# Optimization experiments

Hardware: AMD Instinct MI355X
Metric: run time of the kernel (lower is better)

## Reference

```python
import jax, jax.numpy as jnp
import numpy as np

EMBED_DIMS = 1024
NUM_HEADS = 16
HEAD_DIMS = EMBED_DIMS // NUM_HEADS


def setup_inputs() -> dict:
    key = jax.random.key(0)
    k_x, k_wqkv, k_bqkv, k_wp, k_bp = jax.random.split(key, 5)
    B, N, D = 2, 2048, EMBED_DIMS
    x = jax.random.normal(k_x, (B, N, D), dtype=jnp.float32)
    # torch nn.Linear(in, out): weight [out, in], y = x @ W.T + b
    s = 1.0 / np.sqrt(D)
    W_qkv = jax.random.uniform(k_wqkv, (3 * D, D), jnp.float32, -s, s)
    b_qkv = jax.random.uniform(k_bqkv, (3 * D,), jnp.float32, -s, s)
    W_proj = jax.random.uniform(k_wp, (D, D), jnp.float32, -s, s)
    b_proj = jax.random.uniform(k_bp, (D,), jnp.float32, -s, s)
    return {"x": x, "W_qkv": W_qkv, "b_qkv": b_qkv, "W_proj": W_proj, "b_proj": b_proj}


def reference(x, W_qkv, b_qkv, W_proj, b_proj):
    B, N, D = x.shape
    H, Hd = NUM_HEADS, HEAD_DIMS
    # qkv projection: [B, N, 3, H, Hd] -> split q, k, v as [B, H, N, Hd]
    qkv = (x @ W_qkv.T + b_qkv).reshape(B, N, 3, H, Hd).transpose(2, 0, 3, 1, 4)
    q, k, v = qkv[0], qkv[1], qkv[2]
    scale = 1.0 / jnp.sqrt(jnp.asarray(Hd, x.dtype))
    attn = jnp.einsum("bhqd,bhkd->bhqk", q, k) * scale  # [B, H, N, N]
    attn = jax.nn.softmax(attn, axis=-1)
    out = jnp.einsum("bhqk,bhkd->bhqd", attn, v)  # [B, H, N, Hd]
    out = out.transpose(0, 2, 1, 3).reshape(B, N, D)
    out = out @ W_proj.T + b_proj
    return out
```

## Files before the change

### kernel.cpp

```cpp
#include <hip/hip_runtime.h>

typedef _Float16 f16x8 __attribute__((ext_vector_type(8)));
typedef __attribute__((ext_vector_type(4))) float f32x4;

static __device__ __forceinline__ unsigned short f2h(float f) {
  return __builtin_bit_cast(unsigned short, (_Float16)f);
}

#if __has_builtin(__builtin_amdgcn_exp2f)
#define EXP2(x) __builtin_amdgcn_exp2f(x)
#else
#define EXP2(x) exp2f(x)
#endif

#define GLOAD_LDS16(gp, lp)                                          \
  __builtin_amdgcn_global_load_lds(                                  \
      (const __attribute__((address_space(1))) unsigned int*)(gp),   \
      (__attribute__((address_space(3))) unsigned int*)(lp), 16, 0, 0)

__global__ __launch_bounds__(256) void cvt_all(
    const float* __restrict__ X, const float* __restrict__ Wq,
    const float* __restrict__ Wp, unsigned short* __restrict__ Xb,
    unsigned short* __restrict__ Wqb, unsigned short* __restrict__ Wpb) {
  const int i = blockIdx.x * 256 + threadIdx.x;
  const float4* src;
  unsigned short* dst;
  int off;
  if (i < 1048576) {
    src = (const float4*)X; dst = Xb; off = i;
  } else if (i < 1835008) {
    src = (const float4*)Wq; dst = Wqb; off = i - 1048576;
  } else {
    src = (const float4*)Wp; dst = Wpb; off = i - 1835008;
  }
  const float4 v = src[off];
  *(ushort4*)(dst + (size_t)off * 4) =
      make_ushort4(f2h(v.x), f2h(v.y), f2h(v.z), f2h(v.w));
}

__global__ __launch_bounds__(512) void qkv_gemm(
    const unsigned short* __restrict__ Xb, const unsigned short* __restrict__ Wb,
    const float* __restrict__ bias, unsigned short* __restrict__ Qb,
    unsigned short* __restrict__ Kb, unsigned short* __restrict__ Vt) {
  __shared__ __align__(16) unsigned short A_sh[2][128 * 32];
  __shared__ __align__(16) unsigned short B_sh[2][128 * 32];
  const int n0 = blockIdx.x * 128, m0 = blockIdx.y * 128;
  const int tid = threadIdx.x, lane = tid & 63, wave = tid >> 6;
  const int wr = wave >> 1, wc = wave & 1;
  const int lm = lane & 15, lg = lane >> 4;
  const int r4 = lane >> 2;
  const int sg8 = (((lane & 3) ^ ((r4 >> 1) & 3)) * 8);
  const int lgx = (lg ^ ((lm >> 1) & 3)) * 8;

  f32x4 acc[2][4] = {};

#define QSTAGE(k0_, b_)                                                       \
  do {                                                                        \
    if (wave < 4) {                                                           \
      _Pragma("unroll")                                                       \
      for (int j = 0; j < 2; ++j) {                                           \
        const int chunk = wave * 2 + j;                                       \
        const int row = chunk * 16 + r4;                                      \
        GLOAD_LDS16(Xb + (size_t)(m0 + row) * 1024 + (k0_) + sg8,             \
                    &A_sh[b_][chunk * 512]);                                  \
      }                                                                       \
    } else {                                                                  \
      _Pragma("unroll")                                                       \
      for (int j = 0; j < 2; ++j) {                                           \
        const int chunk = (wave - 4) * 2 + j;                                 \
        const int row = chunk * 16 + r4;                                      \
        GLOAD_LDS16(Wb + (size_t)(n0 + row) * 1024 + (k0_) + sg8,             \
                    &B_sh[b_][chunk * 512]);                                  \
      }                                                                       \
    }                                                                         \
  } while (0)

  QSTAGE(0, 0);

  for (int it = 0; it < 32; ++it) {
    const int cur = it & 1;
    __syncthreads();
    if (it < 31) QSTAGE((it + 1) * 32, cur ^ 1);

    f16x8 af[2], bfr[4];
#pragma unroll
    for (int mi = 0; mi < 2; ++mi)
      af[mi] = *(const f16x8*)&A_sh[cur][(wr * 32 + mi * 16 + lm) * 32 + lgx];
#pragma unroll
    for (int ni = 0; ni < 4; ++ni)
      bfr[ni] = *(const f16x8*)&B_sh[cur][(wc * 64 + ni * 16 + lm) * 32 + lgx];
#pragma unroll
    for (int mi = 0; mi < 2; ++mi)
#pragma unroll
      for (int ni = 0; ni < 4; ++ni)
        acc[mi][ni] = __builtin_amdgcn_mfma_f32_16x16x32_f16(
            af[mi], bfr[ni], acc[mi][ni], 0, 0, 0);
  }
#undef QSTAGE

  const float qscale = 0.18033688011112042f;
#pragma unroll
  for (int mi = 0; mi < 2; ++mi) {
#pragma unroll
    for (int ni = 0; ni < 4; ++ni) {
      const int gn = n0 + wc * 64 + ni * 16 + lm;
      const float bv = bias[gn];
      const int which = gn >> 10;
      const int h = (gn >> 6) & 15;
      const int hd = gn & 63;
      float v[4];
#pragma unroll
      for (int r = 0; r < 4; ++r) v[r] = acc[mi][ni][r] + bv;
      const int gm0 = m0 + wr * 32 + mi * 16 + lg * 4;
      const int bb = gm0 >> 11;
      const int nq0 = gm0 & 2047;
      if (which == 0) {
        unsigned short* p = Qb + (((size_t)bb * 16 + h) * 2048 + nq0) * 64 + hd;
        p[0] = f2h(v[0] * qscale);   p[64] = f2h(v[1] * qscale);
        p[128] = f2h(v[2] * qscale); p[192] = f2h(v[3] * qscale);
      } else if (which == 1) {
        unsigned short* p = Kb + (((size_t)bb * 16 + h) * 2048 + nq0) * 64 + hd;
        p[0] = f2h(v[0]);   p[64] = f2h(v[1]);
        p[128] = f2h(v[2]); p[192] = f2h(v[3]);
      } else {
        *(ushort4*)(Vt + (((size_t)bb * 16 + h) * 64 + hd) * 2048 + nq0) =
            make_ushort4(f2h(v[0]), f2h(v[1]), f2h(v[2]), f2h(v[3]));
      }
    }
  }
}

__global__ __launch_bounds__(512) void attn_kernel(
    const unsigned short* __restrict__ Qb, const unsigned short* __restrict__ Kb,
    const unsigned short* __restrict__ Vt, unsigned short* __restrict__ Ob) {
  __shared__ __align__(16) unsigned short K_sh[2][2][64 * 32];
  __shared__ __align__(16) unsigned short V_sh[2][2][64 * 32];
  __shared__ __align__(16) unsigned short P_sh[128 * 68];
  const int bh = blockIdx.y, q0 = blockIdx.x * 128;
  const size_t base = (size_t)bh * (2048 * 64);
  const unsigned short* Qp = Qb + base;
  const unsigned short* Kp = Kb + base;
  const unsigned short* Vp = Vt + base;
  const int tid = threadIdx.x, lane = tid & 63, wave = tid >> 6;
  const int lm = lane & 15, lg = lane >> 4;
  const int r4 = lane >> 2;
  const int sg8 = (((lane & 3) ^ ((r4 >> 1) & 3)) * 8);
  const int lgx = (lg ^ ((lm >> 1) & 3)) * 8;

  f16x8 qf[2];
#pragma unroll
  for (int kc = 0; kc < 2; ++kc)
    qf[kc] = *(const f16x8*)(Qp +
        (size_t)(q0 + wave * 16 + lm) * 64 + kc * 32 + lg * 8);

  f32x4 o[4] = {};
  float lsum[4] = {};

  const bool isV = wave >= 4;
  const int plane = wave & 1;
  const int half = (wave >> 1) & 1;

#define STAGE(kt_, b_)                                                        \
  do {                                                                        \
    if (!isV) {                                                               \
      _Pragma("unroll")                                                       \
      for (int qv = 0; qv < 2; ++qv)                                          \
        GLOAD_LDS16(Kp + (size_t)((kt_) * 64 + half * 32 + qv * 16 + r4) * 64 \
                        + plane * 32 + sg8,                                   \
                    &K_sh[b_][plane][(half * 2 + qv) * 512]);                 \
    } else {                                                                  \
      _Pragma("unroll")                                                       \
      for (int qv = 0; qv < 2; ++qv)                                          \
        GLOAD_LDS16(Vp + (size_t)(half * 32 + qv * 16 + r4) * 2048 +          \
                        (kt_) * 64 + plane * 32 + sg8,                        \
                    &V_sh[b_][plane][(half * 2 + qv) * 512]);                 \
    }                                                                         \
  } while (0)

  STAGE(0, 0);

  for (int kt = 0; kt < 32; ++kt) {
    const int cur = kt & 1;
    __syncthreads();
    if (kt < 31) STAGE(kt + 1, cur ^ 1);

    f32x4 s[4] = {};
#pragma unroll
    for (int kc = 0; kc < 2; ++kc) {
#pragma unroll
      for (int ni = 0; ni < 4; ++ni) {
        const f16x8 kf =
            *(const f16x8*)&K_sh[cur][kc][(ni * 16 + lm) * 32 + lgx];
        s[ni] = __builtin_amdgcn_mfma_f32_16x16x32_f16(qf[kc], kf, s[ni], 0, 0, 0);
      }
    }

#pragma unroll
    for (int ni = 0; ni < 4; ++ni) {
      float p0 = EXP2(s[ni][0]), p1 = EXP2(s[ni][1]);
      float p2 = EXP2(s[ni][2]), p3 = EXP2(s[ni][3]);
      lsum[0] += p0; lsum[1] += p1; lsum[2] += p2; lsum[3] += p3;
      unsigned short* pp = &P_sh[(wave * 16 + lg * 4) * 68 + ni * 16 + lm];
      pp[0] = f2h(p0);    pp[68] = f2h(p1);
      pp[136] = f2h(p2);  pp[204] = f2h(p3);
    }

#pragma unroll
    for (int kc = 0; kc < 2; ++kc) {
      const f16x8 pa =
          *(const f16x8*)&P_sh[(wave * 16 + lm) * 68 + kc * 32 + lg * 8];
#pragma unroll
      for (int ni = 0; ni < 4; ++ni) {
        const f16x8 vb =
            *(const f16x8*)&V_sh[cur][kc][(ni * 16 + lm) * 32 + lgx];
        o[ni] = __builtin_amdgcn_mfma_f32_16x16x32_f16(pa, vb, o[ni], 0, 0, 0);
      }
    }
  }
#undef STAGE

  const int b = bh >> 4, h = bh & 15;
#pragma unroll
  for (int r = 0; r < 4; ++r) {
    float l = lsum[r];
    l += __shfl_xor(l, 1);
    l += __shfl_xor(l, 2);
    l += __shfl_xor(l, 4);
    l += __shfl_xor(l, 8);
    const float inv = 1.0f / l;
    const int nq = q0 + wave * 16 + lg * 4 + r;
    unsigned short* p = Ob + ((size_t)(b * 2048 + nq) * 16 + h) * 64 + lm;
    p[0] = f2h(o[0][r] * inv);
    p[16] = f2h(o[1][r] * inv);
    p[32] = f2h(o[2][r] * inv);
    p[48] = f2h(o[3][r] * inv);
  }
}

__global__ __launch_bounds__(256) void proj_gemm(
    const unsigned short* __restrict__ A, const unsigned short* __restrict__ Wb,
    const float* __restrict__ bias, float* __restrict__ Out) {
  __shared__ __align__(16) unsigned short A_sh[2][64 * 32];
  __shared__ __align__(16) unsigned short B_sh[2][128 * 32];
  const int n0 = blockIdx.x * 128, m0 = blockIdx.y * 64;
  const int tid = threadIdx.x, lane = tid & 63, wave = tid >> 6;
  const int wr = wave >> 1, wc = wave & 1, lm = lane & 15, lg = lane >> 4;
  const int r4 = lane >> 2;
  const int sg8 = (((lane & 3) ^ ((r4 >> 1) & 3)) * 8);
  const int lgx = (lg ^ ((lm >> 1) & 3)) * 8;

  f32x4 acc[2][4] = {};

#define PSTAGE(k0_, b_)                                                       \
  do {                                                                        \
    {                                                                         \
      const int row = wave * 16 + r4;                                         \
      GLOAD_LDS16(A + (size_t)(m0 + row) * 1024 + (k0_) + sg8,                \
                  &A_sh[b_][wave * 512]);                                     \
    }                                                                         \
    _Pragma("unroll")                                                         \
    for (int j = 0; j < 2; ++j) {                                             \
      const int chunk = wave * 2 + j;                                         \
      const int row = chunk * 16 + r4;                                        \
      GLOAD_LDS16(Wb + (size_t)(n0 + row) * 1024 + (k0_) + sg8,               \
                  &B_sh[b_][chunk * 512]);                                    \
    }                                                                         \
  } while (0)

  PSTAGE(0, 0);

  for (int it = 0; it < 32; ++it) {
    const int cur = it & 1;
    __syncthreads();
    if (it < 31) PSTAGE((it + 1) * 32, cur ^ 1);

    f16x8 af[2], bfr[4];
#pragma unroll
    for (int mi = 0; mi < 2; ++mi)
      af[mi] = *(const f16x8*)&A_sh[cur][(wr * 32 + mi * 16 + lm) * 32 + lgx];
#pragma unroll
    for (int ni = 0; ni < 4; ++ni)
      bfr[ni] = *(const f16x8*)&B_sh[cur][(wc * 64 + ni * 16 + lm) * 32 + lgx];
#pragma unroll
    for (int mi = 0; mi < 2; ++mi)
#pragma unroll
      for (int ni = 0; ni < 4; ++ni)
        acc[mi][ni] = __builtin_amdgcn_mfma_f32_16x16x32_f16(
            af[mi], bfr[ni], acc[mi][ni], 0, 0, 0);
  }
#undef PSTAGE

#pragma unroll
  for (int mi = 0; mi < 2; ++mi)
#pragma unroll
    for (int ni = 0; ni < 4; ++ni) {
      const int gn = n0 + wc * 64 + ni * 16 + lm;
      const float bv = bias[gn];
#pragma unroll
      for (int r = 0; r < 4; ++r) {
        const int gm = m0 + wr * 32 + mi * 16 + lg * 4 + r;
        Out[(size_t)gm * 1024 + gn] = acc[mi][ni][r] + bv;
      }
    }
}

extern "C" void kernel_launch(void* const* d_in, const int* in_sizes, int n_in,
                              void* d_out, int out_size, void* d_ws, size_t ws_size,
                              hipStream_t stream) {
  const float* x      = (const float*)d_in[0];
  const float* W_qkv  = (const float*)d_in[1];
  const float* b_qkv  = (const float*)d_in[2];
  const float* W_proj = (const float*)d_in[3];
  const float* b_proj = (const float*)d_in[4];
  float* out = (float*)d_out;

  unsigned short* Qb  = (unsigned short*)d_ws;
  unsigned short* Kb  = Qb + 4194304;
  unsigned short* Vt  = Kb + 4194304;
  unsigned short* Ao  = Vt + 4194304;
  unsigned short* Xb  = Ao + 4194304;
  unsigned short* Wqb = Xb + 4194304;
  unsigned short* Wpb = Wqb + 3145728;

  cvt_all<<<8192, 256, 0, stream>>>(x, W_qkv, W_proj, Xb, Wqb, Wpb);
  qkv_gemm<<<dim3(24, 32), 512, 0, stream>>>(Xb, Wqb, b_qkv, Qb, Kb, Vt);
  attn_kernel<<<dim3(16, 32), 512, 0, stream>>>(Qb, Kb, Vt, Ao);
  proj_gemm<<<dim3(8, 64), 256, 0, stream>>>(Ao, Wpb, b_proj, out);
}
```

Before: 195.2 us.

## Give each attention wave two 16-row Q tiles to reuse K/V fragments

The attention kernel moves from 8 waves with one 16-row query tile each to 4 waves with two tiles each. K and V fragments are loaded once from LDS and reused across both tiles, halving LDS reads per MFMA. P is now written and consumed in two 32-column phases through a smaller P buffer, and s_setprio is raised around the MFMA clusters. The trade-off is fewer waves per block to hide latency, higher register pressure, and each wave issuing twice as many K/V staging loads.

```diff
diff --git a/kernel.cpp b/kernel.cpp
--- a/kernel.cpp
+++ b/kernel.cpp
@@ -130,12 +130,12 @@
   }
 }
 
-__global__ __launch_bounds__(512) void attn_kernel(
+__global__ __launch_bounds__(256) void attn_kernel(
     const unsigned short* __restrict__ Qb, const unsigned short* __restrict__ Kb,
     const unsigned short* __restrict__ Vt, unsigned short* __restrict__ Ob) {
   __shared__ __align__(16) unsigned short K_sh[2][2][64 * 32];
   __shared__ __align__(16) unsigned short V_sh[2][2][64 * 32];
-  __shared__ __align__(16) unsigned short P_sh[128 * 68];
+  __shared__ __align__(16) unsigned short P_sh[128 * 36];
   const int bh = blockIdx.y, q0 = blockIdx.x * 128;
   const size_t base = (size_t)bh * (2048 * 64);
   const unsigned short* Qp = Qb + base;
@@ -147,33 +147,34 @@
   const int sg8 = (((lane & 3) ^ ((r4 >> 1) & 3)) * 8);
   const int lgx = (lg ^ ((lm >> 1) & 3)) * 8;
 
-  f16x8 qf[2];
-#pragma unroll
-  for (int kc = 0; kc < 2; ++kc)
-    qf[kc] = *(const f16x8*)(Qp +
-        (size_t)(q0 + wave * 16 + lm) * 64 + kc * 32 + lg * 8);
-
-  f32x4 o[4] = {};
-  float lsum[4] = {};
-
-  const bool isV = wave >= 4;
+  f16x8 qf[2][2];
+#pragma unroll
+  for (int mi = 0; mi < 2; ++mi)
+#pragma unroll
+    for (int kc = 0; kc < 2; ++kc)
+      qf[mi][kc] = *(const f16x8*)(Qp +
+          (size_t)(q0 + wave * 32 + mi * 16 + lm) * 64 + kc * 32 + lg * 8);
+
+  f32x4 o[2][4] = {};
+  float lsum[2][4] = {};
+
+  const bool isV = wave >= 2;
   const int plane = wave & 1;
-  const int half = (wave >> 1) & 1;
 
 #define STAGE(kt_, b_)                                                        \
   do {                                                                        \
     if (!isV) {                                                               \
       _Pragma("unroll")                                                       \
-      for (int qv = 0; qv < 2; ++qv)                                          \
-        GLOAD_LDS16(Kp + (size_t)((kt_) * 64 + half * 32 + qv * 16 + r4) * 64 \
-                        + plane * 32 + sg8,                                   \
-                    &K_sh[b_][plane][(half * 2 + qv) * 512]);                 \
+      for (int c = 0; c < 4; ++c)                                             \
+        GLOAD_LDS16(Kp + (size_t)((kt_) * 64 + c * 16 + r4) * 64 +            \
+                        plane * 32 + sg8,                                     \
+                    &K_sh[b_][plane][c * 512]);                               \
     } else {                                                                  \
       _Pragma("unroll")                                                       \
-      for (int qv = 0; qv < 2; ++qv)                                          \
-        GLOAD_LDS16(Vp + (size_t)(half * 32 + qv * 16 + r4) * 2048 +          \
+      for (int c = 0; c < 4; ++c)                                             \
+        GLOAD_LDS16(Vp + (size_t)(c * 16 + r4) * 2048 +                       \
                         (kt_) * 64 + plane * 32 + sg8,                        \
-                    &V_sh[b_][plane][(half * 2 + qv) * 512]);                 \
+                    &V_sh[b_][plane][c * 512]);                               \
     }                                                                         \
   } while (0)
 
@@ -184,57 +185,84 @@
     __syncthreads();
     if (kt < 31) STAGE(kt + 1, cur ^ 1);
 
-    f32x4 s[4] = {};
-#pragma unroll
-    for (int kc = 0; kc < 2; ++kc) {
+    f16x8 kfr[2][4];
+#pragma unroll
+    for (int kc = 0; kc < 2; ++kc)
+#pragma unroll
+      for (int ni = 0; ni < 4; ++ni)
+        kfr[kc][ni] =
+            *(const f16x8*)&K_sh[cur][kc][(ni * 16 + lm) * 32 + lgx];
+
+    f32x4 s[2][4] = {};
+    __builtin_amdgcn_s_setprio(1);
+#pragma unroll
+    for (int kc = 0; kc < 2; ++kc)
 #pragma unroll
       for (int ni = 0; ni < 4; ++ni) {
-        const f16x8 kf =
-            *(const f16x8*)&K_sh[cur][kc][(ni * 16 + lm) * 32 + lgx];
-        s[ni] = __builtin_amdgcn_mfma_f32_16x16x32_f16(qf[kc], kf, s[ni], 0, 0, 0);
+        s[0][ni] = __builtin_amdgcn_mfma_f32_16x16x32_f16(
+            qf[0][kc], kfr[kc][ni], s[0][ni], 0, 0, 0);
+        s[1][ni] = __builtin_amdgcn_mfma_f32_16x16x32_f16(
+            qf[1][kc], kfr[kc][ni], s[1][ni], 0, 0, 0);
       }
+    __builtin_amdgcn_s_setprio(0);
+
+#pragma unroll
+    for (int ph = 0; ph < 2; ++ph) {
+#pragma unroll
+      for (int mi = 0; mi < 2; ++mi)
+#pragma unroll
+        for (int nn = 0; nn < 2; ++nn) {
+          const f32x4 sv = s[mi][ph * 2 + nn];
+          float e0 = EXP2(sv[0]), e1 = EXP2(sv[1]);
+          float e2 = EXP2(sv[2]), e3 = EXP2(sv[3]);
+          lsum[mi][0] += e0; lsum[mi][1] += e1;
+          lsum[mi][2] += e2; lsum[mi][3] += e3;
+          unsigned short* pp =
+              &P_sh[(wave * 32 + mi * 16 + lg * 4) * 36 + nn * 16 + lm];
+          pp[0] = f2h(e0);   pp[36] = f2h(e1);
+          pp[72] = f2h(e2);  pp[108] = f2h(e3);
+        }
+
+      f16x8 pa[2], vbr[4];
+#pragma unroll
+      for (int mi = 0; mi < 2; ++mi)
+        pa[mi] =
+            *(const f16x8*)&P_sh[(wave * 32 + mi * 16 + lm) * 36 + lg * 8];
+#pragma unroll
+      for (int ni = 0; ni < 4; ++ni)
+        vbr[ni] =
+            *(const f16x8*)&V_sh[cur][ph][(ni * 16 + lm) * 32 + lgx];
+      __builtin_amdgcn_s_setprio(1);
+#pragma unroll
+      for (int ni = 0; ni < 4; ++ni) {
+        o[0][ni] = __builtin_amdgcn_mfma_f32_16x16x32_f16(
+            pa[0], vbr[ni], o[0][ni], 0, 0, 0);
+        o[1][ni] = __builtin_amdgcn_mfma_f32_16x16x32_f16(
+            pa[1], vbr[ni], o[1][ni], 0, 0, 0);
+      }
+      __builtin_amdgcn_s_setprio(0);
     }
-
-#pragma unroll
-    for (int ni = 0; ni < 4; ++ni) {
-      float p0 = EXP2(s[ni][0]), p1 = EXP2(s[ni][1]);
-      float p2 = EXP2(s[ni][2]), p3 = EXP2(s[ni][3]);
-      lsum[0] += p0; lsum[1] += p1; lsum[2] += p2; lsum[3] += p3;
-      unsigned short* pp = &P_sh[(wave * 16 + lg * 4) * 68 + ni * 16 + lm];
-      pp[0] = f2h(p0);    pp[68] = f2h(p1);
-      pp[136] = f2h(p2);  pp[204] = f2h(p3);
+  }
+#undef STAGE
+
+  const int b = bh >> 4, h = bh & 15;
+#pragma unroll
+  for (int mi = 0; mi < 2; ++mi)
+#pragma unroll
+    for (int r = 0; r < 4; ++r) {
+      float l = lsum[mi][r];
+      l += __shfl_xor(l, 1);
+      l += __shfl_xor(l, 2);
+      l += __shfl_xor(l, 4);
+      l += __shfl_xor(l, 8);
+      const float inv = 1.0f / l;
+      const int nq = q0 + wave * 32 + mi * 16 + lg * 4 + r;
+      unsigned short* p = Ob + ((size_t)(b * 2048 + nq) * 16 + h) * 64 + lm;
+      p[0] = f2h(o[mi][0][r] * inv);
+      p[16] = f2h(o[mi][1][r] * inv);
+      p[32] = f2h(o[mi][2][r] * inv);
+      p[48] = f2h(o[mi][3][r] * inv);
     }
-
-#pragma unroll
-    for (int kc = 0; kc < 2; ++kc) {
-      const f16x8 pa =
-          *(const f16x8*)&P_sh[(wave * 16 + lm) * 68 + kc * 32 + lg * 8];
-#pragma unroll
-      for (int ni = 0; ni < 4; ++ni) {
-        const f16x8 vb =
-            *(const f16x8*)&V_sh[cur][kc][(ni * 16 + lm) * 32 + lgx];
-        o[ni] = __builtin_amdgcn_mfma_f32_16x16x32_f16(pa, vb, o[ni], 0, 0, 0);
-      }
-    }
-  }
-#undef STAGE
-
-  const int b = bh >> 4, h = bh & 15;
-#pragma unroll
-  for (int r = 0; r < 4; ++r) {
-    float l = lsum[r];
-    l += __shfl_xor(l, 1);
-    l += __shfl_xor(l, 2);
-    l += __shfl_xor(l, 4);
-    l += __shfl_xor(l, 8);
-    const float inv = 1.0f / l;
-    const int nq = q0 + wave * 16 + lg * 4 + r;
-    unsigned short* p = Ob + ((size_t)(b * 2048 + nq) * 16 + h) * 64 + lm;
-    p[0] = f2h(o[0][r] * inv);
-    p[16] = f2h(o[1][r] * inv);
-    p[32] = f2h(o[2][r] * inv);
-    p[48] = f2h(o[3][r] * inv);
-  }
 }
 
 __global__ __launch_bounds__(256) void proj_gemm(
@@ -324,6 +352,6 @@
 
   cvt_all<<<8192, 256, 0, stream>>>(x, W_qkv, W_proj, Xb, Wqb, Wpb);
   qkv_gemm<<<dim3(24, 32), 512, 0, stream>>>(Xb, Wqb, b_qkv, Qb, Kb, Vt);
-  attn_kernel<<<dim3(16, 32), 512, 0, stream>>>(Qb, Kb, Vt, Ao);
+  attn_kernel<<<dim3(16, 32), 256, 0, stream>>>(Qb, Kb, Vt, Ao);
   proj_gemm<<<dim3(8, 64), 256, 0, stream>>>(Ao, Wpb, b_proj, out);
 }
```

Result: slower. 200.0 us (+2.5%).
